# Performance work log

Measured on AMD Instinct MI355X. Metric: run time of the kernel, lower is better.

The kernel has to match this reference:

```python
import jax, jax.numpy as jnp
import numpy as np

DIM = 192; D_STATE = 16; D_CONV = 4; EXPAND = 2
D_INNER = EXPAND * DIM          # 384
DT_RANK = -(-DIM // 16)         # ceil(192/16) = 12
BSZ, T, H, W = 1, 16, 64, 64


def setup_inputs() -> dict:
    key = jax.random.key(0)
    ks = jax.random.split(key, 10)
    s = 0.02
    return {
        "x": jax.random.normal(ks[0], (BSZ, DIM, T, H, W), jnp.float32),
        "ln1_g": jnp.ones((DIM,), jnp.float32),
        "ln1_b": jnp.zeros((DIM,), jnp.float32),
        "ln2_g": jnp.ones((DIM,), jnp.float32),
        "ln2_b": jnp.zeros((DIM,), jnp.float32),
        "W_in": jax.random.normal(ks[1], (2 * D_INNER, DIM), jnp.float32) * s,
        "conv_w": jax.random.normal(ks[2], (D_INNER, D_CONV), jnp.float32) * 0.3,
        "conv_b": jnp.zeros((D_INNER,), jnp.float32),
        "W_xp": jax.random.normal(ks[3], (DT_RANK + 2 * D_STATE, D_INNER), jnp.float32) * s,
        "W_dt": jax.random.normal(ks[4], (D_INNER, DT_RANK), jnp.float32) * 0.1,
        "b_dt": jax.random.normal(ks[5], (D_INNER,), jnp.float32) * 0.1 - 4.0,
        "A_log": jnp.log(jnp.broadcast_to(jnp.arange(1, D_STATE + 1, dtype=jnp.float32), (D_INNER, D_STATE))),
        "D": jnp.ones((D_INNER,), jnp.float32),
        "W_out": jax.random.normal(ks[6], (DIM, D_INNER), jnp.float32) * s,
    }


def _layer_norm(x, g, b, eps=1e-5):
    m = x.mean(-1, keepdims=True)
    v = ((x - m) ** 2).mean(-1, keepdims=True)
    return (x - m) * jax.lax.rsqrt(v + eps) * g + b


def _mamba(tokens, W_in, conv_w, conv_b, W_xp, W_dt, b_dt, A_log, D, W_out):
    B, L, _ = tokens.shape
    xz = tokens @ W_in.T                      # (B, L, 2*d_inner)
    xc, z = jnp.split(xz, 2, axis=-1)
    # causal depthwise conv1d along L
    xin = xc.transpose(0, 2, 1)               # (B, d_inner, L)
    xconv = jax.lax.conv_general_dilated(
        xin, conv_w[:, None, :], (1,), [(D_CONV - 1, 0)],
        dimension_numbers=("NCH", "OIH", "NCH"), feature_group_count=D_INNER)
    xconv = xconv + conv_b[None, :, None]
    xs = jax.nn.silu(xconv.transpose(0, 2, 1))  # (B, L, d_inner)
    x_dbl = xs @ W_xp.T                        # (B, L, dt_rank + 2*d_state)
    dt, Bm, Cm = jnp.split(x_dbl, [DT_RANK, DT_RANK + D_STATE], axis=-1)
    dt = jax.nn.softplus(dt @ W_dt.T + b_dt)   # (B, L, d_inner)
    A = -jnp.exp(A_log)                        # (d_inner, d_state)
    dA = jnp.exp(dt[..., None] * A)            # (B, L, d_inner, d_state)
    dBx = dt[..., None] * Bm[:, :, None, :] * xs[..., None]

    def step(h, inp):
        dA_t, dBx_t, C_t = inp
        h = dA_t * h + dBx_t                   # (B, d_inner, d_state)
        return h, jnp.einsum("bds,bs->bd", h, C_t)

    h0 = jnp.zeros((B, D_INNER, D_STATE), tokens.dtype)
    _, ys = jax.lax.scan(step, h0, (dA.transpose(1, 0, 2, 3),
                                    dBx.transpose(1, 0, 2, 3),
                                    Cm.transpose(1, 0, 2)))
    y = ys.transpose(1, 0, 2) + xs * D         # (B, L, d_inner)
    y = y * jax.nn.silu(z)
    return y @ W_out.T                          # (B, L, dim)


def reference(x, ln1_g, ln1_b, ln2_g, ln2_b, W_in, conv_w, conv_b,
              W_xp, W_dt, b_dt, A_log, D, W_out):
    B, C, T_, H_, W_ = x.shape
    Hs, Ws = H_ // 4, W_ // 4
    # avg_pool3d kernel=(1,4,4) stride=(1,4,4)
    x_ds = x.reshape(B, C, T_, Hs, 4, Ws, 4).mean((4, 6))
    tokens = x_ds.reshape(B, C, T_ * Hs * Ws).transpose(0, 2, 1)  # (B, L, C)
    y = _layer_norm(tokens, ln1_g, ln1_b)
    y = _mamba(y, W_in, conv_w, conv_b, W_xp, W_dt, b_dt, A_log, D, W_out)
    out = _layer_norm(tokens + y, ln2_g, ln2_b)                    # (B, L, C)
    out5 = out.transpose(0, 2, 1).reshape(B, C, T_, Hs, Ws)
    pooled = out5.mean((3, 4))                                     # (B, C, T)
    mag = jnp.abs(jnp.fft.rfft(pooled, axis=2))
    weight = jax.nn.sigmoid(mag[:, :, 1:8].mean(-1))               # (B, C)
    out5 = out5 * weight[:, :, None, None, None]
    up = jax.image.resize(out5, (B, C, T_, H_, W_), method="trilinear")
    return up * jax.nn.sigmoid(x)
```

## Files before the change

kernel.cpp:

```cpp
#include <hip/hip_runtime.h>
#include <math.h>

#define DIMC 192
#define DI   384
#define DS   16
#define LTOK 4096
#define NCH  256
#define CLEN 16
#define NLANE (DI*DS)
#define L2E  1.4426950408889634f
#define LN2  0.6931471805599453f

typedef __attribute__((ext_vector_type(8))) short    bf16x8;
typedef __attribute__((ext_vector_type(8))) unsigned short u16x8;
typedef __attribute__((ext_vector_type(4))) float    f32x4;

__device__ __forceinline__ float EXP2(float x) { return __builtin_amdgcn_exp2f(x); }
__device__ __forceinline__ float RCP(float x)  { return __builtin_amdgcn_rcpf(x); }
__device__ __forceinline__ float LOG2(float x) { return __builtin_amdgcn_logf(x); }

__device__ __forceinline__ float sigmoidf_(float x) { return RCP(1.f + EXP2(-x * L2E)); }
__device__ __forceinline__ float siluf_(float x)    { return x * RCP(1.f + EXP2(-x * L2E)); }
__device__ __forceinline__ unsigned short f2bf(float f) {
    unsigned int u = __float_as_uint(f);
    u += 0x7FFFu + ((u >> 16) & 1u);
    return (unsigned short)(u >> 16);
}
__device__ __forceinline__ float bf2f(unsigned short b) {
    return __uint_as_float(((unsigned int)b) << 16);
}

__global__ __launch_bounds__(256) void poolln_kernel(const float* __restrict__ x,
                                                     const float* __restrict__ g,
                                                     const float* __restrict__ bb,
                                                     const float* __restrict__ W_in,
                                                     const float* __restrict__ W_out,
                                                     const float* __restrict__ W_xp,
                                                     const float* __restrict__ A_log,
                                                     float* __restrict__ tokens,
                                                     unsigned short* __restrict__ ytok,
                                                     unsigned short* __restrict__ W_in_bf,
                                                     unsigned short* __restrict__ W_out_bf,
                                                     unsigned short* __restrict__ W_xp_pad,
                                                     float* __restrict__ A2pre) {
    int blk = blockIdx.x;
    int tid = threadIdx.x;
    if (blk >= 256) {
        int id = (blk - 256) * 256 + tid;
        for (int i = id; i < 768 * 192; i += 8192) W_in_bf[i] = f2bf(W_in[i]);
        for (int i = id; i < 192 * 384; i += 8192) W_out_bf[i] = f2bf(W_out[i]);
        for (int i = id; i < 64 * 384; i += 8192) {
            int row = i / 384;
            W_xp_pad[i] = (row < 44) ? f2bf(W_xp[i]) : (unsigned short)0;
        }
        for (int i = id; i < NLANE; i += 8192) A2pre[i] = -expf(A_log[i]) * L2E;
        return;
    }
    int t = blk >> 4, hs = blk & 15;
    int grp = tid >> 4, ws = tid & 15;
    __shared__ float P[16 * 196];
    __shared__ float ms[16], rs[16];
    #pragma unroll
    for (int k = 0; k < 12; ++k) {
        int c = grp + (k << 4);
        const float* base = x + ((size_t)(c * 16 + t) * 64 + hs * 4) * 64 + ws * 4;
        float s = 0.f;
        #pragma unroll
        for (int i = 0; i < 4; ++i) {
            float4 v = *(const float4*)(base + i * 64);
            s += v.x + v.y + v.z + v.w;
        }
        P[ws * 196 + c] = s * 0.0625f;
    }
    __syncthreads();
    float s1 = 0.f, s2 = 0.f;
    #pragma unroll
    for (int k = 0; k < 12; ++k) {
        float v = P[grp * 196 + ws + 16 * k];
        s1 += v; s2 += v * v;
    }
    s1 += __shfl_xor(s1, 1); s2 += __shfl_xor(s2, 1);
    s1 += __shfl_xor(s1, 2); s2 += __shfl_xor(s2, 2);
    s1 += __shfl_xor(s1, 4); s2 += __shfl_xor(s2, 4);
    s1 += __shfl_xor(s1, 8); s2 += __shfl_xor(s2, 8);
    if (ws == 0) {
        float m = s1 * (1.f / 192.f);
        ms[grp] = m;
        rs[grp] = rsqrtf(s2 * (1.f / 192.f) - m * m + 1e-5f);
    }
    __syncthreads();
    int l0 = t * 256 + hs * 16;
    for (int e = tid; e < 16 * 192; e += 256) {
        int w2 = e / 192, c = e - w2 * 192;
        float v = P[w2 * 196 + c];
        float val = (v - ms[w2]) * rs[w2] * g[c] + bb[c];
        tokens[(size_t)(l0 + w2) * DIMC + c] = v;
        ytok[(size_t)(l0 + w2) * DIMC + c] = f2bf(val);
    }
}

template<int K>
__global__ __launch_bounds__(256) void gemm_mfma(const unsigned short* __restrict__ A,
                                                 const unsigned short* __restrict__ Wb,
                                                 float* __restrict__ Cout,
                                                 int N) {
    constexpr int KP = K + 8;
    __shared__ unsigned short As[64 * KP];
    __shared__ unsigned short Bs[64 * KP];
    int bm = blockIdx.y * 64;
    int bn = blockIdx.x * 64;
    int tid = threadIdx.x;
    for (int c = tid; c < 64 * (K / 8); c += 256) {
        int row = c / (K / 8), col = (c % (K / 8)) * 8;
        *(u16x8*)&As[row * KP + col] = *(const u16x8*)(A + (size_t)(bm + row) * K + col);
        *(u16x8*)&Bs[row * KP + col] = *(const u16x8*)(Wb + (size_t)(bn + row) * K + col);
    }
    __syncthreads();
    int lane = tid & 63, w = tid >> 6;
    int wr = w >> 1, wc = w & 1;
    int r16 = lane & 15, h = lane >> 4;
    f32x4 acc[2][2] = {};
    #pragma unroll
    for (int k0 = 0; k0 < K; k0 += 32) {
        bf16x8 a0 = *(const bf16x8*)&As[(wr * 32 + r16)      * KP + k0 + 8 * h];
        bf16x8 a1 = *(const bf16x8*)&As[(wr * 32 + 16 + r16) * KP + k0 + 8 * h];
        bf16x8 b0 = *(const bf16x8*)&Bs[(wc * 32 + r16)      * KP + k0 + 8 * h];
        bf16x8 b1 = *(const bf16x8*)&Bs[(wc * 32 + 16 + r16) * KP + k0 + 8 * h];
        acc[0][0] = __builtin_amdgcn_mfma_f32_16x16x32_bf16(a0, b0, acc[0][0], 0, 0, 0);
        acc[0][1] = __builtin_amdgcn_mfma_f32_16x16x32_bf16(a0, b1, acc[0][1], 0, 0, 0);
        acc[1][0] = __builtin_amdgcn_mfma_f32_16x16x32_bf16(a1, b0, acc[1][0], 0, 0, 0);
        acc[1][1] = __builtin_amdgcn_mfma_f32_16x16x32_bf16(a1, b1, acc[1][1], 0, 0, 0);
    }
    #pragma unroll
    for (int fm = 0; fm < 2; ++fm)
        #pragma unroll
        for (int fn = 0; fn < 2; ++fn)
            #pragma unroll
            for (int i = 0; i < 4; ++i) {
                int r = bm + wr * 32 + fm * 16 + h * 4 + i;
                int cc = bn + wc * 32 + fn * 16 + r16;
                Cout[(size_t)r * N + cc] = acc[fm][fn][i];
            }
}

__global__ __launch_bounds__(256) void convxdbl(const float* __restrict__ xz,
                                                const float* __restrict__ conv_w,
                                                const float* __restrict__ conv_b,
                                                const unsigned short* __restrict__ Wxp,
                                                unsigned short* __restrict__ xsb,
                                                float* __restrict__ x_dbl) {
    int l0 = blockIdx.x * 16;
    int tid = threadIdx.x;
    __shared__ unsigned short As[16 * 392];
    __shared__ float xd[16 * 64];
    for (int e = tid * 2; e < 16 * 384; e += 512) {
        int row = e / 384, d = e - row * 384;
        int l = l0 + row;
        float ax = conv_b[d], ay = conv_b[d + 1];
        #pragma unroll
        for (int k = 0; k < 4; ++k) {
            int ll = l - 3 + k;
            if (ll >= 0) {
                float2 v = *(const float2*)(xz + (size_t)ll * 768 + d);
                ax = fmaf(conv_w[d * 4 + k],       v.x, ax);
                ay = fmaf(conv_w[(d + 1) * 4 + k], v.y, ay);
            }
        }
        ushort2 b2;
        b2.x = f2bf(siluf_(ax));
        b2.y = f2bf(siluf_(ay));
        *(ushort2*)&As[row * 392 + d] = b2;
        *(ushort2*)(xsb + (size_t)l * 384 + d) = b2;
    }
    __syncthreads();
    int lane = tid & 63, w = tid >> 6;
    int r16 = lane & 15, hh = lane >> 4;
    f32x4 acc = {};
    #pragma unroll
    for (int k0 = 0; k0 < 384; k0 += 32) {
        bf16x8 a = *(const bf16x8*)&As[r16 * 392 + k0 + 8 * hh];
        bf16x8 b = *(const bf16x8*)(Wxp + (size_t)(w * 16 + r16) * 384 + k0 + 8 * hh);
        acc = __builtin_amdgcn_mfma_f32_16x16x32_bf16(a, b, acc, 0, 0, 0);
    }
    #pragma unroll
    for (int i = 0; i < 4; ++i) xd[(hh * 4 + i) * 64 + w * 16 + r16] = acc[i];
    __syncthreads();
    {
        int e = tid * 4;
        int row = e >> 6, col = e & 63;
        *(float4*)(x_dbl + (size_t)(l0 + row) * 64 + col) = *(const float4*)&xd[e];
    }
}

__global__ __launch_bounds__(256) void scan1(const float* __restrict__ x_dbl,
                                             const unsigned short* __restrict__ xsb,
                                             const float* __restrict__ W_dt,
                                             const float* __restrict__ b_dt,
                                             const float* __restrict__ A2pre,
                                             float* __restrict__ chA,
                                             float* __restrict__ chB,
                                             float* __restrict__ Dloc,
                                             unsigned short* __restrict__ yloc) {
    int tid = threadIdx.x;
    int dg = blockIdx.x;
    int c  = blockIdx.y;
    __shared__ float xdblS[16 * 48];
    __shared__ float wdtS[64 * 13];
    __shared__ float dtS[16][64];
    __shared__ unsigned short xsS[16][64];
    for (int i = tid; i < 768; i += 256) {
        int row = i / 48, col = i - row * 48;
        xdblS[i] = x_dbl[(size_t)(c * 16 + row) * 64 + col];
    }
    for (int i = tid; i < 768; i += 256) {
        int dl_ = i / 12, r = i - dl_ * 12;
        wdtS[dl_ * 13 + r] = W_dt[(size_t)dg * 768 + i];
    }
    for (int i = tid; i < 1024; i += 256) {
        int row = i >> 6, dl_ = i & 63;
        xsS[row][dl_] = xsb[(size_t)(c * 16 + row) * 384 + dg * 64 + dl_];
    }
    __syncthreads();
    {
        int dl_ = tid & 63;
        float bd = b_dt[dg * 64 + dl_];
        #pragma unroll
        for (int i2 = 0; i2 < 4; ++i2) {
            int row = (tid >> 6) + 4 * i2;
            float s = bd;
            #pragma unroll
            for (int r = 0; r < 12; ++r)
                s = fmaf(xdblS[row * 48 + r], wdtS[dl_ * 13 + r], s);
            dtS[row][dl_] = (s > 20.f) ? s : LOG2(1.f + EXP2(s * L2E)) * LN2;
        }
    }
    __syncthreads();
    int sq = tid & 3, dl = tid >> 2;
    int d = dg * 64 + dl;
    float4 a4 = *(const float4*)(A2pre + (size_t)d * DS + sq * 4);
    float A2[4] = {a4.x, a4.y, a4.z, a4.w};
    float h[4] = {};
    float dts = 0.f;
    #pragma unroll
    for (int i = 0; i < CLEN; ++i) {
        int l = c * CLEN + i;
        float dtv = dtS[i][dl];
        float xv  = bf2f(xsS[i][dl]);
        float dtx = dtv * xv;
        dts += dtv;
        float y = 0.f;
        #pragma unroll
        for (int u = 0; u < 4; ++u) {
            float a = EXP2(dtv * A2[u]);
            h[u] = fmaf(a, h[u], dtx * xdblS[i * 48 + 12 + sq * 4 + u]);
            y = fmaf(h[u], xdblS[i * 48 + 28 + sq * 4 + u], y);
        }
        y += __shfl_xor(y, 1);
        y += __shfl_xor(y, 2);
        if (sq == 0) {
            yloc[(size_t)l * DI + d] = f2bf(y);
            Dloc[(size_t)l * DI + d] = dts;
        }
    }
    size_t base = (size_t)c * NLANE + d * DS + sq * 4;
    float4 pa, pb;
    pa.x = EXP2(dts * A2[0]); pa.y = EXP2(dts * A2[1]);
    pa.z = EXP2(dts * A2[2]); pa.w = EXP2(dts * A2[3]);
    pb.x = h[0]; pb.y = h[1]; pb.z = h[2]; pb.w = h[3];
    *(float4*)&chA[base] = pa;
    *(float4*)&chB[base] = pb;
}

__global__ __launch_bounds__(256) void scan2(const float* __restrict__ chA,
                                             const float* __restrict__ chB,
                                             float* __restrict__ hst) {
    int lane = blockIdx.x * 256 + threadIdx.x;
    float h = 0.f;
    for (int c0 = 0; c0 < NCH; c0 += 8) {
        float a[8], b[8];
        #pragma unroll
        for (int u = 0; u < 8; ++u) {
            a[u] = chA[(size_t)(c0 + u) * NLANE + lane];
            b[u] = chB[(size_t)(c0 + u) * NLANE + lane];
        }
        #pragma unroll
        for (int u = 0; u < 8; ++u) {
            hst[(size_t)(c0 + u) * NLANE + lane] = h;
            h = fmaf(a[u], h, b[u]);
        }
    }
}

__global__ __launch_bounds__(256) void scan3fix(const float* __restrict__ hst,
                                                const float* __restrict__ Dloc,
                                                const float* __restrict__ x_dbl,
                                                const float* __restrict__ A2pre,
                                                const unsigned short* __restrict__ xsb,
                                                const float* __restrict__ xz,
                                                const float* __restrict__ Dvec,
                                                unsigned short* __restrict__ ybuf) {
    int dg = blockIdx.x;
    int c  = blockIdx.y;
    int tid = threadIdx.x;
    int ll = tid >> 4, dl = tid & 15;
    int d = dg * 16 + dl;
    int l = c * 16 + ll;
    __shared__ float hpS[16][17];
    __shared__ float A2S[16][17];
    __shared__ float CsS[256];
    {
        int dd = tid >> 4, ss = tid & 15;
        hpS[dd][ss] = hst[(size_t)c * NLANE + dg * 256 + tid];
        A2S[dd][ss] = A2pre[(size_t)dg * 256 + tid];
        CsS[tid]    = x_dbl[(size_t)(c * 16 + dd) * 64 + 28 + ss];
    }
    __syncthreads();
    float Dl = Dloc[(size_t)l * DI + d];
    float y  = bf2f(ybuf[(size_t)l * DI + d]);
    float xv = bf2f(xsb[(size_t)l * DI + d]);
    float z  = xz[(size_t)l * 768 + 384 + d];
    #pragma unroll
    for (int s = 0; s < 16; ++s) {
        float e = EXP2(A2S[dl][s] * Dl);
        y = fmaf(CsS[ll * 16 + s] * e, hpS[dl][s], y);
    }
    float val = (y + xv * Dvec[d]) * siluf_(z);
    ybuf[(size_t)l * DI + d] = f2bf(val);
}

__global__ __launch_bounds__(256) void ln2_kernel(const float* __restrict__ tokens,
                                                  const float* __restrict__ gout,
                                                  const float* __restrict__ g,
                                                  const float* __restrict__ bb,
                                                  float* __restrict__ o5) {
    int blk = blockIdx.x;
    int t = blk >> 4, g16 = blk & 15;
    int l0 = t * 256 + g16 * 16;
    int tid = threadIdx.x;
    __shared__ float P[16 * 196];
    __shared__ float ms[16], rs[16];
    for (int e = tid; e < 3072; e += 256) {
        int w2 = e / 192, c = e - w2 * 192;
        size_t off = (size_t)(l0 + w2) * DIMC + c;
        P[w2 * 196 + c] = tokens[off] + gout[off];
    }
    __syncthreads();
    int grp = tid >> 4, ws = tid & 15;
    float s1 = 0.f, s2 = 0.f;
    #pragma unroll
    for (int k = 0; k < 12; ++k) {
        float v = P[grp * 196 + ws + 16 * k];
        s1 += v; s2 += v * v;
    }
    s1 += __shfl_xor(s1, 1); s2 += __shfl_xor(s2, 1);
    s1 += __shfl_xor(s1, 2); s2 += __shfl_xor(s2, 2);
    s1 += __shfl_xor(s1, 4); s2 += __shfl_xor(s2, 4);
    s1 += __shfl_xor(s1, 8); s2 += __shfl_xor(s2, 8);
    if (ws == 0) {
        float m = s1 * (1.f / 192.f);
        ms[grp] = m;
        rs[grp] = rsqrtf(s2 * (1.f / 192.f) - m * m + 1e-5f);
    }
    __syncthreads();
    for (int e = tid; e < 3072; e += 256) {
        int c = e >> 4, w2 = e & 15;
        float val = (P[w2 * 196 + c] - ms[w2]) * rs[w2] * g[c] + bb[c];
        o5[((size_t)c * 16 + t) * 256 + g16 * 16 + w2] = val;
    }
}

__global__ __launch_bounds__(256) void fft_kernel(const float* __restrict__ o5,
                                                  float* __restrict__ wgt) {
    int c = blockIdx.x;
    __shared__ float pooled[16];
    __shared__ float mag[8];
    int tid = threadIdx.x;
    int wv = tid >> 6, lane = tid & 63;
    for (int t = wv * 4; t < wv * 4 + 4; ++t) {
        float s = 0.f;
        #pragma unroll
        for (int r = 0; r < 4; ++r) s += o5[(size_t)c * 4096 + t * 256 + lane + r * 64];
        s += __shfl_xor(s, 1); s += __shfl_xor(s, 2); s += __shfl_xor(s, 4);
        s += __shfl_xor(s, 8); s += __shfl_xor(s, 16); s += __shfl_xor(s, 32);
        if (lane == 0) pooled[t] = s * (1.f / 256.f);
    }
    __syncthreads();
    if (tid >= 1 && tid <= 7) {
        int k = tid;
        float re = 0.f, im = 0.f;
        for (int t = 0; t < 16; ++t) {
            float ang = -0.39269908169872414f * (float)(k * t);
            re = fmaf(pooled[t], cosf(ang), re);
            im = fmaf(pooled[t], sinf(ang), im);
        }
        mag[k] = sqrtf(re * re + im * im);
    }
    __syncthreads();
    if (tid == 0) {
        float m = 0.f;
        for (int k = 1; k <= 7; ++k) m += mag[k];
        wgt[c] = sigmoidf_(m * (1.f / 7.f));
    }
}

__global__ __launch_bounds__(256) void upsample_kernel(const float* __restrict__ o5,
                                                       const float* __restrict__ wgt,
                                                       const float* __restrict__ x,
                                                       float* __restrict__ out) {
    int idx = blockIdx.x * 256 + threadIdx.x;
    int k  = idx & 15;
    int h  = (idx >> 4) & 63;
    int t  = (idx >> 10) & 15;
    int c  = idx >> 14;
    float sh = h * 0.25f - 0.375f;
    int h0 = (int)floorf(sh); float fh = sh - (float)h0;
    int h0c = min(max(h0, 0), 15), h1c = min(max(h0 + 1, 0), 15);
    const float* pl = o5 + ((size_t)c * 16 + t) * 256;
    int cm = max(k - 1, 0), cp = min(k + 1, 15);
    float r0m = pl[h0c * 16 + cm], r00 = pl[h0c * 16 + k], r0p = pl[h0c * 16 + cp];
    float r1m = pl[h1c * 16 + cm], r10 = pl[h1c * 16 + k], r1p = pl[h1c * 16 + cp];
    float gh = 1.f - fh;
    float vm = r0m * gh + r1m * fh;
    float v0 = r00 * gh + r10 * fh;
    float vp = r0p * gh + r1p * fh;
    float wc = wgt[c];
    size_t off = (size_t)idx * 4;
    float4 xv = *(const float4*)(x + off);
    float4 o;
    o.x = (vm * 0.375f + v0 * 0.625f) * wc * sigmoidf_(xv.x);
    o.y = (vm * 0.125f + v0 * 0.875f) * wc * sigmoidf_(xv.y);
    o.z = (v0 * 0.875f + vp * 0.125f) * wc * sigmoidf_(xv.z);
    o.w = (v0 * 0.625f + vp * 0.375f) * wc * sigmoidf_(xv.w);
    *(float4*)(out + off) = o;
}

extern "C" void kernel_launch(void* const* d_in, const int* in_sizes, int n_in,
                              void* d_out, int out_size, void* d_ws, size_t ws_size,
                              hipStream_t stream) {
    const float* x      = (const float*)d_in[0];
    const float* ln1_g  = (const float*)d_in[1];
    const float* ln1_b  = (const float*)d_in[2];
    const float* ln2_g  = (const float*)d_in[3];
    const float* ln2_b  = (const float*)d_in[4];
    const float* W_in   = (const float*)d_in[5];
    const float* conv_w = (const float*)d_in[6];
    const float* conv_b = (const float*)d_in[7];
    const float* W_xp   = (const float*)d_in[8];
    const float* W_dt   = (const float*)d_in[9];
    const float* b_dt   = (const float*)d_in[10];
    const float* A_log  = (const float*)d_in[11];
    const float* Dvec   = (const float*)d_in[12];
    const float* W_out  = (const float*)d_in[13];
    float* out = (float*)d_out;

    float* ws = (float*)d_ws;
    float* tokens = ws;  ws += (size_t)LTOK * DIMC;
    float* xz     = ws;  ws += (size_t)LTOK * 768;
    float* x_dbl  = ws;  ws += (size_t)LTOK * 64;
    float* chA    = ws;  ws += (size_t)NLANE * NCH;
    float* chB    = ws;  ws += (size_t)NLANE * NCH;
    float* hst    = ws;  ws += (size_t)NLANE * NCH;
    float* Dloc   = ws;  ws += (size_t)LTOK * DI;
    float* gout   = ws;  ws += (size_t)LTOK * DIMC;
    float* o5     = ws;  ws += (size_t)DIMC * LTOK;
    float* A2pre  = ws;  ws += NLANE;
    float* wgt    = ws;  ws += 256;
    unsigned short* ytok     = (unsigned short*)ws;  ws += (size_t)LTOK * DIMC / 2;
    unsigned short* ybuf     = (unsigned short*)ws;  ws += (size_t)LTOK * DI / 2;
    unsigned short* xsb      = (unsigned short*)ws;  ws += (size_t)LTOK * DI / 2;
    unsigned short* W_in_bf  = (unsigned short*)ws;  ws += (size_t)768 * 192 / 2;
    unsigned short* W_out_bf = (unsigned short*)ws;  ws += (size_t)192 * 384 / 2;
    unsigned short* W_xp_pad = (unsigned short*)ws;  ws += (size_t)64 * 384 / 2;

    poolln_kernel<<<288, 256, 0, stream>>>(x, ln1_g, ln1_b, W_in, W_out, W_xp, A_log,
                                           tokens, ytok, W_in_bf, W_out_bf, W_xp_pad, A2pre);
    gemm_mfma<192><<<dim3(12, 64), 256, 0, stream>>>(ytok, W_in_bf, xz, 768);
    convxdbl<<<256, 256, 0, stream>>>(xz, conv_w, conv_b, W_xp_pad, xsb, x_dbl);
    scan1<<<dim3(6, NCH), 256, 0, stream>>>(x_dbl, xsb, W_dt, b_dt, A2pre, chA, chB, Dloc, ybuf);
    scan2<<<NLANE / 256, 256, 0, stream>>>(chA, chB, hst);
    scan3fix<<<dim3(24, NCH), 256, 0, stream>>>(hst, Dloc, x_dbl, A2pre, xsb, xz, Dvec, ybuf);
    gemm_mfma<384><<<dim3(3, 64), 256, 0, stream>>>(ybuf, W_out_bf, gout, 192);
    ln2_kernel<<<256, 256, 0, stream>>>(tokens, gout, ln2_g, ln2_b, o5);
    fft_kernel<<<192, 256, 0, stream>>>(o5, wgt);
    upsample_kernel<<<12288, 256, 0, stream>>>(o5, wgt, x, out);
}
```

Measured before the change: 124.9 us.

## Parallelize inter-chunk scan across chunks and K-tile the MFMA GEMM

The inter-chunk state scan previously ran one thread per lane serially over 256 chunks in only 24 blocks. It now splits the chunks into 16 groups per lane, composes each group's affine transform, and runs a Hillis-Steele scan in shared memory before the sequential fixup. This launches 384 blocks to fill the GPU, at the cost of extra syncs and multiplies. Separately, the GEMM now loops over K in 192-wide tiles, which shrinks shared memory for the K=384 output projection and may raise occupancy, but adds a sync per tile.

After: 116.0 us. -7.1%, faster.

```diff
diff --git a/kernel.cpp b/kernel.cpp
--- a/kernel.cpp
+++ b/kernel.cpp
@@ -104,32 +104,36 @@
                                                  const unsigned short* __restrict__ Wb,
                                                  float* __restrict__ Cout,
                                                  int N) {
-    constexpr int KP = K + 8;
+    constexpr int KT = 192;
+    constexpr int KP = KT + 8;
     __shared__ unsigned short As[64 * KP];
     __shared__ unsigned short Bs[64 * KP];
     int bm = blockIdx.y * 64;
     int bn = blockIdx.x * 64;
     int tid = threadIdx.x;
-    for (int c = tid; c < 64 * (K / 8); c += 256) {
-        int row = c / (K / 8), col = (c % (K / 8)) * 8;
-        *(u16x8*)&As[row * KP + col] = *(const u16x8*)(A + (size_t)(bm + row) * K + col);
-        *(u16x8*)&Bs[row * KP + col] = *(const u16x8*)(Wb + (size_t)(bn + row) * K + col);
-    }
-    __syncthreads();
     int lane = tid & 63, w = tid >> 6;
     int wr = w >> 1, wc = w & 1;
     int r16 = lane & 15, h = lane >> 4;
     f32x4 acc[2][2] = {};
-    #pragma unroll
-    for (int k0 = 0; k0 < K; k0 += 32) {
-        bf16x8 a0 = *(const bf16x8*)&As[(wr * 32 + r16)      * KP + k0 + 8 * h];
-        bf16x8 a1 = *(const bf16x8*)&As[(wr * 32 + 16 + r16) * KP + k0 + 8 * h];
-        bf16x8 b0 = *(const bf16x8*)&Bs[(wc * 32 + r16)      * KP + k0 + 8 * h];
-        bf16x8 b1 = *(const bf16x8*)&Bs[(wc * 32 + 16 + r16) * KP + k0 + 8 * h];
-        acc[0][0] = __builtin_amdgcn_mfma_f32_16x16x32_bf16(a0, b0, acc[0][0], 0, 0, 0);
-        acc[0][1] = __builtin_amdgcn_mfma_f32_16x16x32_bf16(a0, b1, acc[0][1], 0, 0, 0);
-        acc[1][0] = __builtin_amdgcn_mfma_f32_16x16x32_bf16(a1, b0, acc[1][0], 0, 0, 0);
-        acc[1][1] = __builtin_amdgcn_mfma_f32_16x16x32_bf16(a1, b1, acc[1][1], 0, 0, 0);
+    for (int kt = 0; kt < K; kt += KT) {
+        for (int c = tid; c < 64 * (KT / 8); c += 256) {
+            int row = c / (KT / 8), col = (c % (KT / 8)) * 8;
+            *(u16x8*)&As[row * KP + col] = *(const u16x8*)(A + (size_t)(bm + row) * K + kt + col);
+            *(u16x8*)&Bs[row * KP + col] = *(const u16x8*)(Wb + (size_t)(bn + row) * K + kt + col);
+        }
+        __syncthreads();
+        #pragma unroll
+        for (int k0 = 0; k0 < KT; k0 += 32) {
+            bf16x8 a0 = *(const bf16x8*)&As[(wr * 32 + r16)      * KP + k0 + 8 * h];
+            bf16x8 a1 = *(const bf16x8*)&As[(wr * 32 + 16 + r16) * KP + k0 + 8 * h];
+            bf16x8 b0 = *(const bf16x8*)&Bs[(wc * 32 + r16)      * KP + k0 + 8 * h];
+            bf16x8 b1 = *(const bf16x8*)&Bs[(wc * 32 + 16 + r16) * KP + k0 + 8 * h];
+            acc[0][0] = __builtin_amdgcn_mfma_f32_16x16x32_bf16(a0, b0, acc[0][0], 0, 0, 0);
+            acc[0][1] = __builtin_amdgcn_mfma_f32_16x16x32_bf16(a0, b1, acc[0][1], 0, 0, 0);
+            acc[1][0] = __builtin_amdgcn_mfma_f32_16x16x32_bf16(a1, b0, acc[1][0], 0, 0, 0);
+            acc[1][1] = __builtin_amdgcn_mfma_f32_16x16x32_bf16(a1, b1, acc[1][1], 0, 0, 0);
+        }
+        __syncthreads();
     }
     #pragma unroll
     for (int fm = 0; fm < 2; ++fm)
@@ -271,23 +275,47 @@
     *(float4*)&chB[base] = pb;
 }
 
-__global__ __launch_bounds__(256) void scan2(const float* __restrict__ chA,
-                                             const float* __restrict__ chB,
-                                             float* __restrict__ hst) {
-    int lane = blockIdx.x * 256 + threadIdx.x;
-    float h = 0.f;
-    for (int c0 = 0; c0 < NCH; c0 += 8) {
-        float a[8], b[8];
-        #pragma unroll
-        for (int u = 0; u < 8; ++u) {
-            a[u] = chA[(size_t)(c0 + u) * NLANE + lane];
-            b[u] = chB[(size_t)(c0 + u) * NLANE + lane];
-        }
-        #pragma unroll
-        for (int u = 0; u < 8; ++u) {
-            hst[(size_t)(c0 + u) * NLANE + lane] = h;
-            h = fmaf(a[u], h, b[u]);
-        }
+__global__ __launch_bounds__(256) void scan2p(const float* __restrict__ chA,
+                                              const float* __restrict__ chB,
+                                              float* __restrict__ hst) {
+    int tid = threadIdx.x;
+    int ll = tid & 15;
+    int g  = tid >> 4;
+    int lane = blockIdx.x * 16 + ll;
+    float a[16], b[16];
+    #pragma unroll
+    for (int i = 0; i < 16; ++i) {
+        int c = g * 16 + i;
+        a[i] = chA[(size_t)c * NLANE + lane];
+        b[i] = chB[(size_t)c * NLANE + lane];
+    }
+    float Ath = 1.f, Bth = 0.f;
+    #pragma unroll
+    for (int i = 0; i < 16; ++i) {
+        Bth = fmaf(a[i], Bth, b[i]);
+        Ath *= a[i];
+    }
+    __shared__ float sA[16][17], sB[16][17];
+    sA[g][ll] = Ath; sB[g][ll] = Bth;
+    __syncthreads();
+    #pragma unroll
+    for (int step = 1; step < 16; step <<= 1) {
+        float pA = 1.f, pB = 0.f;
+        if (g >= step) { pA = sA[g - step][ll]; pB = sB[g - step][ll]; }
+        __syncthreads();
+        if (g >= step) {
+            float cA = sA[g][ll], cB = sB[g][ll];
+            sA[g][ll] = cA * pA;
+            sB[g][ll] = fmaf(cA, pB, cB);
+        }
+        __syncthreads();
+    }
+    float h = (g == 0) ? 0.f : sB[g - 1][ll];
+    #pragma unroll
+    for (int i = 0; i < 16; ++i) {
+        int c = g * 16 + i;
+        hst[(size_t)c * NLANE + lane] = h;
+        h = fmaf(a[i], h, b[i]);
     }
 }
 
@@ -477,7 +505,7 @@
     gemm_mfma<192><<<dim3(12, 64), 256, 0, stream>>>(ytok, W_in_bf, xz, 768);
     convxdbl<<<256, 256, 0, stream>>>(xz, conv_w, conv_b, W_xp_pad, xsb, x_dbl);
     scan1<<<dim3(6, NCH), 256, 0, stream>>>(x_dbl, xsb, W_dt, b_dt, A2pre, chA, chB, Dloc, ybuf);
-    scan2<<<NLANE / 256, 256, 0, stream>>>(chA, chB, hst);
+    scan2p<<<NLANE / 16, 256, 0, stream>>>(chA, chB, hst);
     scan3fix<<<dim3(24, NCH), 256, 0, stream>>>(hst, Dloc, x_dbl, A2pre, xsb, xz, Dvec, ybuf);
     gemm_mfma<384><<<dim3(3, 64), 256, 0, stream>>>(ybuf, W_out_bf, gout, 192);
     ln2_kernel<<<256, 256, 0, stream>>>(tokens, gout, ln2_g, ln2_b, o5);
```
